# Kernel tuning notes

Measured on AMD Instinct MI355X. Metric: run time of the kernel, lower is better.

Reference implementation:

```python
import jax, jax.numpy as jnp
import numpy as np

BLOCK = 4096  # bitsandbytes blockwise-quantization block size


def setup_inputs() -> dict:
    key = jax.random.key(0)
    k_x, k_w, k_a, k_c, k_b = jax.random.split(key, 5)
    out_features, in_features = 16384, 4096
    numel = out_features * in_features
    x = jax.random.normal(k_x, (2, 2048, in_features), dtype=jnp.float32)
    # int8 codes stored as indices into the 256-entry dequant table
    qweight = jax.random.randint(k_w, (out_features, in_features), 0, 256, dtype=jnp.int32)
    absmax = jax.random.uniform(k_a, (numel // BLOCK,), dtype=jnp.float32)
    code = jax.random.normal(k_c, (256,), dtype=jnp.float32)
    bias = jax.random.normal(k_b, (out_features,), dtype=jnp.float32)
    return {"x": x, "qweight": qweight, "absmax": absmax, "code": code, "bias": bias}


def reference(x, qweight, absmax, code, bias):
    # dequantize_blockwise: w[i] = code[q[i]] * absmax[i // BLOCK]
    out_f, in_f = qweight.shape
    w = (code[qweight.reshape(-1)].reshape(-1, BLOCK) * absmax[:, None]).reshape(out_f, in_f)
    # F.linear(x, W, b) = x @ W^T + b
    return jnp.einsum("bsi,oi->bso", x, w) + bias
```

## Files before the change

### kernel.cpp

```cpp
#include <hip/hip_runtime.h>
#include <hip/hip_bf16.h>


typedef __bf16 bf16x8 __attribute__((ext_vector_type(8)));
typedef __bf16 bf16x4 __attribute__((ext_vector_type(4)));
typedef float  f32x4  __attribute__((ext_vector_type(4)));

#define GLD_LDS(gp, lp) \
    __builtin_amdgcn_global_load_lds((const __attribute__((address_space(1))) void*)(gp), \
                                     (__attribute__((address_space(3))) void*)(lp), 16, 0, 0)

static constexpr int M = 4096;
static constexpr int N = 16384;
static constexpr int K = 4096;
static constexpr int BM = 128;
static constexpr int BN = 128;
static constexpr int BK = 32;

__global__ __launch_bounds__(256) void dequant_w(const int4* __restrict__ q4,
                                                 const float* __restrict__ code,
                                                 const float* __restrict__ absmax,
                                                 bf16x4* __restrict__ W)
{
    unsigned gid = blockIdx.x * 256u + threadIdx.x;
    int4 qv = q4[gid];
    float am = absmax[gid >> 10];
    bf16x4 w;
    w[0] = (__bf16)(code[qv.x] * am);
    w[1] = (__bf16)(code[qv.y] * am);
    w[2] = (__bf16)(code[qv.z] * am);
    w[3] = (__bf16)(code[qv.w] * am);
    W[gid] = w;
}

__global__ __launch_bounds__(256) void cvt_x(const float4* __restrict__ x,
                                             bf16x4* __restrict__ xb)
{
    unsigned gid = blockIdx.x * 256u + threadIdx.x;
    float4 v = x[gid];
    bf16x4 o;
    o[0] = (__bf16)v.x;
    o[1] = (__bf16)v.y;
    o[2] = (__bf16)v.z;
    o[3] = (__bf16)v.w;
    xb[gid] = o;
}

__global__ __launch_bounds__(256) void gemm_bt_bias(const __bf16* __restrict__ A,
                                                    const __bf16* __restrict__ B,
                                                    const float* __restrict__ bias,
                                                    float* __restrict__ C)
{
    __shared__ __bf16 As[BM * BK];
    __shared__ __bf16 Bs[BN * BK];

    const int tid  = threadIdx.x;
    const int lane = tid & 63;
    const int wave = tid >> 6;
    const int bm = blockIdx.y * BM;
    const int bn = blockIdx.x * BN;
    const int wm = (wave >> 1) * 64;
    const int wn = (wave & 1) * 64;

    const int srow = tid >> 2;
    const int skcol = (tid & 3) * 8;

    const __bf16* ag0 = A + (long long)(bm + srow) * K + skcol;
    const __bf16* bg0 = B + (long long)(bn + srow) * K + skcol;

    f32x4 acc[4][4] = {};

    const int fr = lane & 15;
    const int fk = (lane >> 4) * 8;

    for (int k0 = 0; k0 < K; k0 += BK) {
        __syncthreads();
        GLD_LDS(ag0 + k0,            As + tid * 8);
        GLD_LDS(ag0 + k0 + 64 * K,   As + 2048 + tid * 8);
        GLD_LDS(bg0 + k0,            Bs + tid * 8);
        GLD_LDS(bg0 + k0 + 64 * K,   Bs + 2048 + tid * 8);
        __syncthreads();

        bf16x8 af[4], bfr[4];
#pragma unroll
        for (int i = 0; i < 4; ++i)
            af[i] = *(const bf16x8*)(As + (wm + i * 16 + fr) * BK + fk);
#pragma unroll
        for (int i = 0; i < 4; ++i)
            bfr[i] = *(const bf16x8*)(Bs + (wn + i * 16 + fr) * BK + fk);

#pragma unroll
        for (int mi = 0; mi < 4; ++mi)
#pragma unroll
            for (int ni = 0; ni < 4; ++ni)
                acc[mi][ni] = __builtin_amdgcn_mfma_f32_16x16x32_bf16(
                    af[mi], bfr[ni], acc[mi][ni], 0, 0, 0);
    }

    const int cn = lane & 15;
    const int rq = (lane >> 4) * 4;
#pragma unroll
    for (int ni = 0; ni < 4; ++ni) {
        const int n = bn + wn + ni * 16 + cn;
        const float bv = bias[n];
#pragma unroll
        for (int mi = 0; mi < 4; ++mi) {
#pragma unroll
            for (int r = 0; r < 4; ++r) {
                const int m = bm + wm + mi * 16 + rq + r;
                C[(long long)m * N + n] = acc[mi][ni][r] + bv;
            }
        }
    }
}

extern "C" void kernel_launch(void* const* d_in, const int* in_sizes, int n_in,
                              void* d_out, int out_size, void* d_ws, size_t ws_size,
                              hipStream_t stream)
{
    const float* x      = (const float*)d_in[0];
    const int*   qw     = (const int*)d_in[1];
    const float* absmax = (const float*)d_in[2];
    const float* code   = (const float*)d_in[3];
    const float* bias   = (const float*)d_in[4];
    float* out = (float*)d_out;

    __bf16* Wb = (__bf16*)d_ws;
    __bf16* Xb = (__bf16*)((char*)d_ws + (size_t)N * K * sizeof(__bf16));

    dequant_w<<<(N * (long long)K) / 4 / 256, 256, 0, stream>>>(
        (const int4*)qw, code, absmax, (bf16x4*)Wb);

    cvt_x<<<(M * (long long)K) / 4 / 256, 256, 0, stream>>>(
        (const float4*)x, (bf16x4*)Xb);

    dim3 grid(N / BN, M / BM);
    gemm_bt_bias<<<grid, 256, 0, stream>>>(Xb, Wb, bias, out);
}
```

Baseline: 1.119 ms.

## Use LDS dequant table, swizzle GEMM LDS, group tiles, widen x conversion

The dequant kernel now builds a per-row 256-entry bf16 table in LDS, with the absmax scale prefolded, and looks each code up in that table. This replaces scattered global gathers and multiplies. The GEMM XOR-swizzles the k-chunk position in LDS to reduce bank conflicts on fragment reads, and remaps a 1D grid into 8x16 tile groups for better L2 reuse. The x conversion processes eight floats per thread. Together these touch three kernels and add index arithmetic, and they rely on absmax blocks aligning with rows (K equals BLOCK).

```diff
diff --git a/kernel.cpp b/kernel.cpp
--- a/kernel.cpp
+++ b/kernel.cpp
@@ -17,32 +17,42 @@
 static constexpr int BN = 128;
 static constexpr int BK = 32;
 
-__global__ __launch_bounds__(256) void dequant_w(const int4* __restrict__ q4,
-                                                 const float* __restrict__ code,
-                                                 const float* __restrict__ absmax,
-                                                 bf16x4* __restrict__ W)
+__global__ __launch_bounds__(256) void dequant_w_lds(const int4* __restrict__ q4,
+                                                     const float* __restrict__ code,
+                                                     const float* __restrict__ absmax,
+                                                     uint2* __restrict__ W)
 {
-    unsigned gid = blockIdx.x * 256u + threadIdx.x;
-    int4 qv = q4[gid];
-    float am = absmax[gid >> 10];
-    bf16x4 w;
-    w[0] = (__bf16)(code[qv.x] * am);
-    w[1] = (__bf16)(code[qv.y] * am);
-    w[2] = (__bf16)(code[qv.z] * am);
-    w[3] = (__bf16)(code[qv.w] * am);
-    W[gid] = w;
+    __shared__ unsigned short tab[256];
+    const int o = blockIdx.x;
+    const int t = threadIdx.x;
+    const float am = absmax[o];
+    {
+        __bf16 h = (__bf16)(code[t] * am);
+        tab[t] = __builtin_bit_cast(unsigned short, h);
+    }
+    __syncthreads();
+
+    const int4* row = q4 + (size_t)o * (K / 4);
+    uint2*      out = W  + (size_t)o * (K / 4);
+#pragma unroll
+    for (int i = 0; i < 4; ++i) {
+        const int idx = i * 256 + t;
+        int4 qv = row[idx];
+        unsigned lo = (unsigned)tab[qv.x] | ((unsigned)tab[qv.y] << 16);
+        unsigned hi = (unsigned)tab[qv.z] | ((unsigned)tab[qv.w] << 16);
+        out[idx] = make_uint2(lo, hi);
+    }
 }
 
 __global__ __launch_bounds__(256) void cvt_x(const float4* __restrict__ x,
-                                             bf16x4* __restrict__ xb)
+                                             bf16x8* __restrict__ xb)
 {
     unsigned gid = blockIdx.x * 256u + threadIdx.x;
-    float4 v = x[gid];
-    bf16x4 o;
-    o[0] = (__bf16)v.x;
-    o[1] = (__bf16)v.y;
-    o[2] = (__bf16)v.z;
-    o[3] = (__bf16)v.w;
+    float4 a = x[gid * 2];
+    float4 b = x[gid * 2 + 1];
+    bf16x8 o;
+    o[0] = (__bf16)a.x; o[1] = (__bf16)a.y; o[2] = (__bf16)a.z; o[3] = (__bf16)a.w;
+    o[4] = (__bf16)b.x; o[5] = (__bf16)b.y; o[6] = (__bf16)b.z; o[7] = (__bf16)b.w;
     xb[gid] = o;
 }
 
@@ -57,13 +67,20 @@
     const int tid  = threadIdx.x;
     const int lane = tid & 63;
     const int wave = tid >> 6;
-    const int bm = blockIdx.y * BM;
-    const int bn = blockIdx.x * BN;
+
+    const int id = blockIdx.x;
+    const int g  = id >> 7;
+    const int r  = id & 127;
+    const int gx = g & 15;
+    const int gy = g >> 4;
+    const int bn = (gx * 8  + (r & 7)) * BN;
+    const int bm = (gy * 16 + (r >> 3)) * BM;
+
     const int wm = (wave >> 1) * 64;
     const int wn = (wave & 1) * 64;
 
-    const int srow = tid >> 2;
-    const int skcol = (tid & 3) * 8;
+    const int srow  = tid >> 2;
+    const int skcol = (((tid & 3) ^ ((srow >> 1) & 3))) * 8;
 
     const __bf16* ag0 = A + (long long)(bm + srow) * K + skcol;
     const __bf16* bg0 = B + (long long)(bn + srow) * K + skcol;
@@ -71,7 +88,8 @@
     f32x4 acc[4][4] = {};
 
     const int fr = lane & 15;
-    const int fk = (lane >> 4) * 8;
+    const int fq = lane >> 4;
+    const int fs = (fq ^ ((fr >> 1) & 3)) * 8;
 
     for (int k0 = 0; k0 < K; k0 += BK) {
         __syncthreads();
@@ -84,10 +102,10 @@
         bf16x8 af[4], bfr[4];
 #pragma unroll
         for (int i = 0; i < 4; ++i)
-            af[i] = *(const bf16x8*)(As + (wm + i * 16 + fr) * BK + fk);
+            af[i] = *(const bf16x8*)(As + (wm + i * 16 + fr) * BK + fs);
 #pragma unroll
         for (int i = 0; i < 4; ++i)
-            bfr[i] = *(const bf16x8*)(Bs + (wn + i * 16 + fr) * BK + fk);
+            bfr[i] = *(const bf16x8*)(Bs + (wn + i * 16 + fr) * BK + fs);
 
 #pragma unroll
         for (int mi = 0; mi < 4; ++mi)
@@ -106,9 +124,9 @@
 #pragma unroll
         for (int mi = 0; mi < 4; ++mi) {
 #pragma unroll
-            for (int r = 0; r < 4; ++r) {
-                const int m = bm + wm + mi * 16 + rq + r;
-                C[(long long)m * N + n] = acc[mi][ni][r] + bv;
+            for (int rr = 0; rr < 4; ++rr) {
+                const int m = bm + wm + mi * 16 + rq + rr;
+                C[(long long)m * N + n] = acc[mi][ni][rr] + bv;
             }
         }
     }
@@ -128,12 +146,10 @@
     __bf16* Wb = (__bf16*)d_ws;
     __bf16* Xb = (__bf16*)((char*)d_ws + (size_t)N * K * sizeof(__bf16));
 
-    dequant_w<<<(N * (long long)K) / 4 / 256, 256, 0, stream>>>(
-        (const int4*)qw, code, absmax, (bf16x4*)Wb);
+    dequant_w_lds<<<N, 256, 0, stream>>>((const int4*)qw, code, absmax, (uint2*)Wb);
 
-    cvt_x<<<(M * (long long)K) / 4 / 256, 256, 0, stream>>>(
-        (const float4*)x, (bf16x4*)Xb);
+    cvt_x<<<(M * (long long)K) / 8 / 256, 256, 0, stream>>>(
+        (const float4*)x, (bf16x8*)Xb);
 
-    dim3 grid(N / BN, M / BM);
-    gemm_bt_bias<<<grid, 256, 0, stream>>>(Xb, Wb, bias, out);
+    gemm_bt_bias<<<dim3((M / BM) * (N / BN)), 256, 0, stream>>>(Xb, Wb, bias, out);
 }
```

Result: slower. 1.175 ms (+5.0%).
